# Performance work log

Measured on AMD Instinct MI355X. Metric: run time of the kernel, lower is better.

## Reference

```python
import jax, jax.numpy as jnp
import numpy as np

B, S, D, H = 2, 2048, 1024, 16
HD = D // H  # 64
NUM_BUCKETS = 32
MAX_DISTANCE = 128


def _relative_position_bucket(relative_position, num_buckets=NUM_BUCKETS, max_distance=MAX_DISTANCE):
    # bidirectional=True branch of the torch code
    num_buckets //= 2
    rel_buckets = (relative_position > 0).astype(jnp.int32) * num_buckets
    rp = jnp.abs(relative_position)
    max_exact = num_buckets // 2
    is_small = rp < max_exact
    # log-spaced buckets for larger distances
    rp_large = max_exact + (
        jnp.log(rp.astype(jnp.float32) / max_exact)
        / np.log(max_distance / max_exact)
        * (num_buckets - max_exact)
    ).astype(jnp.int32)
    rp_large = jnp.minimum(rp_large, num_buckets - 1)
    return rel_buckets + jnp.where(is_small, rp, rp_large)


def compute_bias(rel_bias, query_length, key_length):
    ctx = jnp.arange(query_length)[:, None]
    mem = jnp.arange(key_length)[None, :]
    buckets = _relative_position_bucket(mem - ctx)  # [q, k]
    values = rel_bias[buckets]                      # [q, k, h]
    return jnp.transpose(values, (2, 0, 1))[None]   # [1, h, q, k]


def setup_inputs() -> dict:
    key = jax.random.key(0)
    ks = jax.random.split(key, 6)
    scale = 1.0 / np.sqrt(D)
    return {
        "hidden_states": jax.random.normal(ks[0], (B, S, D), jnp.float32),
        "mask": jnp.ones((B, 1, 1, S), jnp.int32),
        "Wq": jax.random.normal(ks[1], (D, D), jnp.float32) * scale,
        "Wk": jax.random.normal(ks[2], (D, D), jnp.float32) * scale,
        "Wv": jax.random.normal(ks[3], (D, D), jnp.float32) * scale,
        "Wo": jax.random.normal(ks[4], (D, D), jnp.float32) * scale,
        "rel_bias": jax.random.normal(ks[5], (NUM_BUCKETS, H), jnp.float32),
    }


def reference(hidden_states, mask, Wq, Wk, Wv, Wo, rel_bias):
    b, s, _ = hidden_states.shape
    # projections (no bias), split heads -> [b, h, s, hd]
    def proj(x, W):
        return jnp.einsum("bsd,ed->bse", x, W).reshape(b, s, H, HD).transpose(0, 2, 1, 3)
    q = proj(hidden_states, Wq)
    k = proj(hidden_states, Wk)
    v = proj(hidden_states, Wv)
    # unscaled attention scores (T5 style): [b, h, s, s]
    scores = jnp.einsum("bhqd,bhkd->bhqk", q, k)
    position_bias = compute_bias(rel_bias, s, s)
    scores = scores + position_bias
    scores = jnp.where(mask == 0, jnp.float32(-1e9), scores)
    attn_weights = jax.nn.softmax(scores, axis=-1)
    # dropout p=0.0 (eval): identity
    attn_output = jnp.einsum("bhqk,bhkd->bhqd", attn_weights, v)
    attn_output = attn_output.transpose(0, 2, 1, 3).reshape(b, s, H * HD)
    attn_output = jnp.einsum("bse,de->bsd", attn_output, Wo)
    return attn_output, attn_weights, position_bias
```

## Files before the change

kernel.cpp:

```cpp
#include <hip/hip_runtime.h>

typedef __attribute__((ext_vector_type(8))) _Float16 half8;
typedef __attribute__((ext_vector_type(4))) _Float16 half4;
typedef __attribute__((ext_vector_type(4))) float f32x4;

#define SEQ 2048
#define DMODEL 1024
#define NHEAD 16
#define HEADD 64
#define NBH 32
#define LUTW 4096

__device__ __forceinline__ void nt_store_f4(float* p, f32x4 v) {
    __builtin_nontemporal_store(v, (f32x4*)p);
}

#define LDS_BAR() do {                                   \
    __builtin_amdgcn_sched_barrier(0);                   \
    asm volatile("s_waitcnt lgkmcnt(0)" ::: "memory");   \
    __builtin_amdgcn_sched_barrier(0);                   \
    __builtin_amdgcn_s_barrier();                        \
    __builtin_amdgcn_sched_barrier(0);                   \
} while (0)

__device__ __forceinline__ int rel_bucket(int rel) {
    int ret = (rel > 0) ? 16 : 0;
    int rp = rel < 0 ? -rel : rel;
    if (rp < 8) return ret + rp;
    float x = logf((float)rp * 0.125f) / 2.7725887f * 8.0f;
    int v = 8 + (int)x;
    v = v < 15 ? v : 15;
    return ret + v;
}

__global__ __launch_bounds__(256) void prep_kernel(const float* __restrict__ hs,
                                                   const float* __restrict__ Wq,
                                                   const float* __restrict__ Wk,
                                                   const float* __restrict__ Wv,
                                                   const float* __restrict__ Wo,
                                                   const float* __restrict__ rel_bias,
                                                   _Float16* __restrict__ Xh,
                                                   _Float16* __restrict__ Wqh,
                                                   _Float16* __restrict__ Wkh,
                                                   _Float16* __restrict__ Wvh,
                                                   _Float16* __restrict__ Woh,
                                                   float* __restrict__ lut) {
    int bid = blockIdx.x;
    if (bid < 4096) {
        const float* in;
        _Float16* out;
        int base;
        if (bid < 2048)      { in = hs; out = Xh;  base = bid; }
        else if (bid < 2560) { in = Wq; out = Wqh; base = bid - 2048; }
        else if (bid < 3072) { in = Wk; out = Wkh; base = bid - 2560; }
        else if (bid < 3584) { in = Wv; out = Wvh; base = bid - 3072; }
        else                 { in = Wo; out = Woh; base = bid - 3584; }
        int i = (base * 256 + threadIdx.x) * 8;
        f32x4 a = *(const f32x4*)(in + i);
        f32x4 b = *(const f32x4*)(in + i + 4);
        half8 r;
        r[0] = (_Float16)a[0]; r[1] = (_Float16)a[1];
        r[2] = (_Float16)a[2]; r[3] = (_Float16)a[3];
        r[4] = (_Float16)b[0]; r[5] = (_Float16)b[1];
        r[6] = (_Float16)b[2]; r[7] = (_Float16)b[3];
        *(half8*)(out + i) = r;
    } else {
        int i = (bid - 4096) * 256 + threadIdx.x;
        int h = i >> 12;
        int idx = i & (LUTW - 1);
        int rel = idx - 2047;
        int b = rel_bucket(rel);
        lut[i] = rel_bias[b * NHEAD + h];
    }
}

__global__ __launch_bounds__(256) void proj3_kernel(const _Float16* __restrict__ Xh,
                                                    const _Float16* __restrict__ Wqh,
                                                    const _Float16* __restrict__ Wkh,
                                                    const _Float16* __restrict__ Wvh,
                                                    _Float16* __restrict__ Qh,
                                                    _Float16* __restrict__ Kh,
                                                    _Float16* __restrict__ Vt,
                                                    const float* __restrict__ lut,
                                                    float* __restrict__ posb) {
    int z = blockIdx.z;
    if (z == 3) {
        int flat = blockIdx.y * 8 + blockIdx.x;
        const size_t total = (size_t)NHEAD * SEQ * SEQ / 4;
        for (size_t idx = (size_t)flat * 256 + threadIdx.x; idx < total; idx += 65536) {
            size_t e = idx * 4;
            int k = (int)(e & 2047);
            int q = (int)((e >> 11) & 2047);
            int h = (int)(e >> 22);
            f32x4 v;
            __builtin_memcpy(&v, lut + h * LUTW + (k - q + 2047), 16);
            nt_store_f4(posb + e, v);
        }
        return;
    }
    const _Float16* B = (z == 0) ? Wqh : (z == 1) ? Wkh : Wvh;
    int l = threadIdx.x & 63, w = threadIdx.x >> 6;
    int row0 = blockIdx.y * 128 + (w >> 1) * 64;
    int col0 = blockIdx.x * 128 + (w & 1) * 64;
    int ar = l & 15, ak = (l >> 4) * 8;
    f32x4 acc[4][4] = {};
    for (int k0 = 0; k0 < DMODEL; k0 += 32) {
        half8 af[4], bf[4];
#pragma unroll
        for (int mi = 0; mi < 4; mi++)
            af[mi] = *(const half8*)(Xh + (size_t)(row0 + mi * 16 + ar) * DMODEL + k0 + ak);
#pragma unroll
        for (int ni = 0; ni < 4; ni++)
            bf[ni] = *(const half8*)(B + (size_t)(col0 + ni * 16 + ar) * DMODEL + k0 + ak);
#pragma unroll
        for (int mi = 0; mi < 4; mi++)
#pragma unroll
            for (int ni = 0; ni < 4; ni++)
                acc[mi][ni] = __builtin_amdgcn_mfma_f32_16x16x32_f16(af[mi], bf[ni], acc[mi][ni], 0, 0, 0);
    }
    int cr = (l >> 4) * 4, cc = l & 15;
    if (z < 2) {
        _Float16* C = z == 0 ? Qh : Kh;
#pragma unroll
        for (int mi = 0; mi < 4; mi++)
#pragma unroll
            for (int ni = 0; ni < 4; ni++) {
                int c = col0 + ni * 16 + cc;
#pragma unroll
                for (int j = 0; j < 4; j++)
                    C[(size_t)(row0 + mi * 16 + cr + j) * DMODEL + c] = (_Float16)acc[mi][ni][j];
            }
    } else {
#pragma unroll
        for (int mi = 0; mi < 4; mi++)
#pragma unroll
            for (int ni = 0; ni < 4; ni++) {
                int c = col0 + ni * 16 + cc;
                int h = c >> 6, hd = c & 63;
                int r = row0 + mi * 16 + cr;
                int b = r >> 11, s0 = r & 2047;
                half4 pk;
#pragma unroll
                for (int j = 0; j < 4; j++) pk[j] = (_Float16)acc[mi][ni][j];
                *(half4*)(Vt + (size_t)((b * NHEAD + h) * HEADD + hd) * SEQ + s0) = pk;
            }
    }
}

__global__ __launch_bounds__(256) void outgemm_kernel(const _Float16* __restrict__ A,
                                                      const _Float16* __restrict__ B,
                                                      float* __restrict__ C) {
    int l = threadIdx.x & 63, w = threadIdx.x >> 6;
    int row0 = blockIdx.y * 128 + (w >> 1) * 64;
    int col0 = blockIdx.x * 128 + (w & 1) * 64;
    int ar = l & 15, ak = (l >> 4) * 8;
    f32x4 acc[4][4] = {};
    for (int k0 = 0; k0 < DMODEL; k0 += 32) {
        half8 af[4], bf[4];
#pragma unroll
        for (int mi = 0; mi < 4; mi++)
            af[mi] = *(const half8*)(A + (size_t)(row0 + mi * 16 + ar) * DMODEL + k0 + ak);
#pragma unroll
        for (int ni = 0; ni < 4; ni++)
            bf[ni] = *(const half8*)(B + (size_t)(col0 + ni * 16 + ar) * DMODEL + k0 + ak);
#pragma unroll
        for (int mi = 0; mi < 4; mi++)
#pragma unroll
            for (int ni = 0; ni < 4; ni++)
                acc[mi][ni] = __builtin_amdgcn_mfma_f32_16x16x32_f16(af[mi], bf[ni], acc[mi][ni], 0, 0, 0);
    }
    int cr = (l >> 4) * 4, cc = l & 15;
#pragma unroll
    for (int mi = 0; mi < 4; mi++)
#pragma unroll
        for (int ni = 0; ni < 4; ni++) {
            int c = col0 + ni * 16 + cc;
#pragma unroll
            for (int j = 0; j < 4; j++)
                C[(size_t)(row0 + mi * 16 + cr + j) * DMODEL + c] = acc[mi][ni][j];
        }
}

__global__ __launch_bounds__(256) void attn_kernel(const _Float16* __restrict__ Q,
                                                   const _Float16* __restrict__ Kg,
                                                   const _Float16* __restrict__ Vg,
                                                   const float* __restrict__ lut,
                                                   const int* __restrict__ mask,
                                                   float* __restrict__ wts,
                                                   _Float16* __restrict__ attn0) {
    __shared__ _Float16 Kt[64][68];
    __shared__ _Float16 Vl[64][68];
    __shared__ _Float16 Pl[4][16][72];
    int tid = threadIdx.x;
    int l = tid & 63, w = tid >> 6;
    int bid = blockIdx.x;
    int xcd = bid & 7, idx = bid >> 3;
    int bh = (idx >> 4) * 8 + xcd;
    int qpair = idx & 15;
    int b = bh >> 4, h = bh & 15;
    int qbaseA = qpair * 64 + w * 16;
    int qbaseB = qbaseA + 1024;
    size_t hoff = (size_t)(b * SEQ) * DMODEL + h * HEADD;
    int ar = l & 15, g = l >> 4, ak = g * 8;
    const float* luth = lut + h * LUTW;
    float* ob = wts + (size_t)bh * SEQ * SEQ;
    int qA = qbaseA + ar;
    int qB = qbaseB + ar;

    int sr = tid >> 2, sc = (tid & 3) * 16;
    const _Float16* Ksrc = Kg + hoff + sc;
    const _Float16* Vsrc = Vg + ((size_t)bh * HEADD + sr) * SEQ + sc;

    half8 qfA[2], qfB[2];
#pragma unroll
    for (int kk = 0; kk < 2; kk++) {
        qfA[kk] = *(const half8*)(Q + hoff + (size_t)qA * DMODEL + kk * 32 + ak);
        qfB[kk] = *(const half8*)(Q + hoff + (size_t)qB * DMODEL + kk * 32 + ak);
    }

    half8 s0 = *(const half8*)(Ksrc + (size_t)sr * DMODEL);
    half8 s1 = *(const half8*)(Ksrc + (size_t)sr * DMODEL + 8);
    float mA = -3e38f, lsumA = 0.f;
    float mB = -3e38f, lsumB = 0.f;
    for (int k0 = 0; k0 < SEQ; k0 += 64) {
        *(half8*)&Kt[sr][sc] = s0;
        *(half8*)&Kt[sr][sc + 8] = s1;
        LDS_BAR();
        if (k0 + 64 < SEQ) {
            s0 = *(const half8*)(Ksrc + (size_t)(k0 + 64 + sr) * DMODEL);
            s1 = *(const half8*)(Ksrc + (size_t)(k0 + 64 + sr) * DMODEL + 8);
        }
        f32x4 accA[4] = {}, accB[4] = {};
#pragma unroll
        for (int ni = 0; ni < 4; ni++)
#pragma unroll
            for (int kk = 0; kk < 2; kk++) {
                half8 kf = *(const half8*)&Kt[ni * 16 + ar][kk * 32 + ak];
                accA[ni] = __builtin_amdgcn_mfma_f32_16x16x32_f16(kf, qfA[kk], accA[ni], 0, 0, 0);
                accB[ni] = __builtin_amdgcn_mfma_f32_16x16x32_f16(kf, qfB[kk], accB[ni], 0, 0, 0);
            }
        LDS_BAR();
        {
            float vv[16];
#pragma unroll
            for (int ni = 0; ni < 4; ni++) {
                int kcol = k0 + ni * 16 + g * 4;
                int4 mk = *(const int4*)(mask + b * SEQ + kcol);
                const int* mp = (const int*)&mk;
                f32x4 lb4;
                __builtin_memcpy(&lb4, luth + kcol - qA + 2047, 16);
#pragma unroll
                for (int j = 0; j < 4; j++)
                    vv[ni * 4 + j] = mp[j] ? (accA[ni][j] + lb4[j]) : -1e9f;
            }
            float t8[8];
#pragma unroll
            for (int t = 0; t < 8; t++) t8[t] = fmaxf(vv[t], vv[t + 8]);
            float t4a = fmaxf(t8[0], t8[4]), t4b = fmaxf(t8[1], t8[5]);
            float t4c = fmaxf(t8[2], t8[6]), t4d = fmaxf(t8[3], t8[7]);
            float vmax = fmaxf(fmaxf(t4a, t4b), fmaxf(t4c, t4d));
            float mn = fmaxf(mA, vmax);
            float scale = __expf(mA - mn);
            float e[16];
#pragma unroll
            for (int t = 0; t < 16; t++) e[t] = __expf(vv[t] - mn);
            float s8[8];
#pragma unroll
            for (int t = 0; t < 8; t++) s8[t] = e[t] + e[t + 8];
            float s4a = s8[0] + s8[4], s4b = s8[1] + s8[5];
            float s4c = s8[2] + s8[6], s4d = s8[3] + s8[7];
            lsumA = lsumA * scale + (s4a + s4b) + (s4c + s4d);
            mA = mn;
        }
        {
            float vv[16];
#pragma unroll
            for (int ni = 0; ni < 4; ni++) {
                int kcol = k0 + ni * 16 + g * 4;
                int4 mk = *(const int4*)(mask + b * SEQ + kcol);
                const int* mp = (const int*)&mk;
                f32x4 lb4;
                __builtin_memcpy(&lb4, luth + kcol - qB + 2047, 16);
#pragma unroll
                for (int j = 0; j < 4; j++)
                    vv[ni * 4 + j] = mp[j] ? (accB[ni][j] + lb4[j]) : -1e9f;
            }
            float t8[8];
#pragma unroll
            for (int t = 0; t < 8; t++) t8[t] = fmaxf(vv[t], vv[t + 8]);
            float t4a = fmaxf(t8[0], t8[4]), t4b = fmaxf(t8[1], t8[5]);
            float t4c = fmaxf(t8[2], t8[6]), t4d = fmaxf(t8[3], t8[7]);
            float vmax = fmaxf(fmaxf(t4a, t4b), fmaxf(t4c, t4d));
            float mn = fmaxf(mB, vmax);
            float scale = __expf(mB - mn);
            float e[16];
#pragma unroll
            for (int t = 0; t < 16; t++) e[t] = __expf(vv[t] - mn);
            float s8[8];
#pragma unroll
            for (int t = 0; t < 8; t++) s8[t] = e[t] + e[t + 8];
            float s4a = s8[0] + s8[4], s4b = s8[1] + s8[5];
            float s4c = s8[2] + s8[6], s4d = s8[3] + s8[7];
            lsumB = lsumB * scale + (s4a + s4b) + (s4c + s4d);
            mB = mn;
        }
    }
    half8 t0 = *(const half8*)(Ksrc + (size_t)sr * DMODEL);
    half8 t1 = *(const half8*)(Ksrc + (size_t)sr * DMODEL + 8);
    half8 v0 = *(const half8*)(Vsrc);
    half8 v1 = *(const half8*)(Vsrc + 8);
#pragma unroll
    for (int off2 = 16; off2 <= 32; off2 <<= 1) {
        float mo = __shfl_xor(mA, off2);
        float lo = __shfl_xor(lsumA, off2);
        float mn = fmaxf(mA, mo);
        lsumA = lsumA * __expf(mA - mn) + lo * __expf(mo - mn);
        mA = mn;
        mo = __shfl_xor(mB, off2);
        lo = __shfl_xor(lsumB, off2);
        mn = fmaxf(mB, mo);
        lsumB = lsumB * __expf(mB - mn) + lo * __expf(mo - mn);
        mB = mn;
    }
    float invlA = 1.0f / lsumA;
    float invlB = 1.0f / lsumB;
    LDS_BAR();

    f32x4 oaccA[4] = {}, oaccB[4] = {};
    for (int k0 = 0; k0 < SEQ; k0 += 64) {
        *(half8*)&Kt[sr][sc] = t0;
        *(half8*)&Kt[sr][sc + 8] = t1;
        *(half8*)&Vl[sr][sc] = v0;
        *(half8*)&Vl[sr][sc + 8] = v1;
        LDS_BAR();
        if (k0 + 64 < SEQ) {
            t0 = *(const half8*)(Ksrc + (size_t)(k0 + 64 + sr) * DMODEL);
            t1 = *(const half8*)(Ksrc + (size_t)(k0 + 64 + sr) * DMODEL + 8);
            v0 = *(const half8*)(Vsrc + k0 + 64);
            v1 = *(const half8*)(Vsrc + k0 + 64 + 8);
        }
        f32x4 accA[4] = {}, accB[4] = {};
#pragma unroll
        for (int ni = 0; ni < 4; ni++)
#pragma unroll
            for (int kk = 0; kk < 2; kk++) {
                half8 kf = *(const half8*)&Kt[ni * 16 + ar][kk * 32 + ak];
                accA[ni] = __builtin_amdgcn_mfma_f32_16x16x32_f16(kf, qfA[kk], accA[ni], 0, 0, 0);
                accB[ni] = __builtin_amdgcn_mfma_f32_16x16x32_f16(kf, qfB[kk], accB[ni], 0, 0, 0);
            }
#pragma unroll
        for (int ni = 0; ni < 4; ni++) {
            int kcol = k0 + ni * 16 + g * 4;
            int4 mk = *(const int4*)(mask + b * SEQ + kcol);
            const int* mp = (const int*)&mk;
            f32x4 lb4;
            __builtin_memcpy(&lb4, luth + kcol - qA + 2047, 16);
            f32x4 wv;
#pragma unroll
            for (int j = 0; j < 4; j++) {
                float v = mp[j] ? (accA[ni][j] + lb4[j]) : -1e9f;
                wv[j] = __expf(v - mA) * invlA;
            }
            nt_store_f4(ob + (size_t)qA * SEQ + kcol, wv);
            half4 ph;
#pragma unroll
            for (int j = 0; j < 4; j++) ph[j] = (_Float16)wv[j];
            *(half4*)&Pl[w][ar][ni * 16 + g * 4] = ph;
        }
#pragma unroll
        for (int kk2 = 0; kk2 < 2; kk2++) {
            half8 pa = *(half8*)&Pl[w][ar][kk2 * 32 + g * 8];
#pragma unroll
            for (int ni = 0; ni < 4; ni++) {
                half8 vf = *(const half8*)&Vl[ni * 16 + ar][kk2 * 32 + g * 8];
                oaccA[ni] = __builtin_amdgcn_mfma_f32_16x16x32_f16(pa, vf, oaccA[ni], 0, 0, 0);
            }
        }
#pragma unroll
        for (int ni = 0; ni < 4; ni++) {
            int kcol = k0 + ni * 16 + g * 4;
            int4 mk = *(const int4*)(mask + b * SEQ + kcol);
            const int* mp = (const int*)&mk;
            f32x4 lb4;
            __builtin_memcpy(&lb4, luth + kcol - qB + 2047, 16);
            f32x4 wv;
#pragma unroll
            for (int j = 0; j < 4; j++) {
                float v = mp[j] ? (accB[ni][j] + lb4[j]) : -1e9f;
                wv[j] = __expf(v - mB) * invlB;
            }
            nt_store_f4(ob + (size_t)qB * SEQ + kcol, wv);
            half4 ph;
#pragma unroll
            for (int j = 0; j < 4; j++) ph[j] = (_Float16)wv[j];
            *(half4*)&Pl[w][ar][ni * 16 + g * 4] = ph;
        }
#pragma unroll
        for (int kk2 = 0; kk2 < 2; kk2++) {
            half8 pa = *(half8*)&Pl[w][ar][kk2 * 32 + g * 8];
#pragma unroll
            for (int ni = 0; ni < 4; ni++) {
                half8 vf = *(const half8*)&Vl[ni * 16 + ar][kk2 * 32 + g * 8];
                oaccB[ni] = __builtin_amdgcn_mfma_f32_16x16x32_f16(pa, vf, oaccB[ni], 0, 0, 0);
            }
        }
        LDS_BAR();
    }
#pragma unroll
    for (int ni = 0; ni < 4; ni++)
#pragma unroll
        for (int j = 0; j < 4; j++) {
            attn0[(size_t)(b * SEQ + qbaseA + g * 4 + j) * DMODEL + h * HEADD + ni * 16 + ar] =
                (_Float16)oaccA[ni][j];
            attn0[(size_t)(b * SEQ + qbaseB + g * 4 + j) * DMODEL + h * HEADD + ni * 16 + ar] =
                (_Float16)oaccB[ni][j];
        }
}

extern "C" void kernel_launch(void* const* d_in, const int* in_sizes, int n_in,
                              void* d_out, int out_size, void* d_ws, size_t ws_size,
                              hipStream_t stream) {
    const float* hs = (const float*)d_in[0];
    const int* mask = (const int*)d_in[1];
    const float* Wq = (const float*)d_in[2];
    const float* Wk = (const float*)d_in[3];
    const float* Wv = (const float*)d_in[4];
    const float* Wo = (const float*)d_in[5];
    const float* rel_bias = (const float*)d_in[6];

    float* out_attn = (float*)d_out;
    float* out_wts = out_attn + (size_t)2 * SEQ * DMODEL;
    float* out_posb = out_wts + (size_t)NBH * SEQ * SEQ;

    char* ws = (char*)d_ws;
    size_t off = 0;
    auto carve = [&](size_t bytes) { void* p = ws + off; off += (bytes + 255) & ~(size_t)255; return p; };
    _Float16* Xh  = (_Float16*)carve((size_t)2 * SEQ * DMODEL * 2);
    _Float16* Wqh = (_Float16*)carve((size_t)DMODEL * DMODEL * 2);
    _Float16* Wkh = (_Float16*)carve((size_t)DMODEL * DMODEL * 2);
    _Float16* Wvh = (_Float16*)carve((size_t)DMODEL * DMODEL * 2);
    _Float16* Woh = (_Float16*)carve((size_t)DMODEL * DMODEL * 2);
    _Float16* Qh  = (_Float16*)carve((size_t)2 * SEQ * DMODEL * 2);
    _Float16* Kh  = (_Float16*)carve((size_t)2 * SEQ * DMODEL * 2);
    _Float16* Vt  = (_Float16*)carve((size_t)NBH * HEADD * SEQ * 2);
    _Float16* A0h = (_Float16*)carve((size_t)2 * SEQ * DMODEL * 2);
    float* lut    = (float*)carve((size_t)NHEAD * LUTW * 4);

    prep_kernel<<<4352, 256, 0, stream>>>(hs, Wq, Wk, Wv, Wo, rel_bias,
                                          Xh, Wqh, Wkh, Wvh, Woh, lut);

    dim3 pg(DMODEL / 128, (2 * SEQ) / 128, 4);
    proj3_kernel<<<pg, 256, 0, stream>>>(Xh, Wqh, Wkh, Wvh, Qh, Kh, Vt, lut, out_posb);

    attn_kernel<<<512, 256, 0, stream>>>(Qh, Kh, Vt, lut, mask, out_wts, A0h);

    dim3 og(DMODEL / 128, (2 * SEQ) / 128);
    outgemm_kernel<<<og, 256, 0, stream>>>(A0h, Woh, out_attn);
}
```

Baseline: 433.6 us.

## Merge two query-pair blocks into one 512-thread block sharing K/V tiles

The attention kernel now launches 256 blocks of 512 threads instead of 512 blocks of 256. Each block covers two query-pair groups that share the same K and V LDS tiles, which halves the global-to-LDS staging per block and splits each thread's load into a single half8. Mask and position-bias loads are also hoisted right after the barrier so they overlap the QK MFMAs. The trade-offs are fewer blocks in the grid for occupancy and higher register pressure under the 512-thread launch bound.

```diff
diff --git a/kernel.cpp b/kernel.cpp
--- a/kernel.cpp
+++ b/kernel.cpp
@@ -181,7 +181,7 @@
         }
 }
 
-__global__ __launch_bounds__(256) void attn_kernel(const _Float16* __restrict__ Q,
+__global__ __launch_bounds__(512) void attn_kernel(const _Float16* __restrict__ Q,
                                                    const _Float16* __restrict__ Kg,
                                                    const _Float16* __restrict__ Vg,
                                                    const float* __restrict__ lut,
@@ -190,15 +190,16 @@
                                                    _Float16* __restrict__ attn0) {
     __shared__ _Float16 Kt[64][68];
     __shared__ _Float16 Vl[64][68];
-    __shared__ _Float16 Pl[4][16][72];
+    __shared__ _Float16 Pl[8][16][72];
     int tid = threadIdx.x;
-    int l = tid & 63, w = tid >> 6;
+    int l = tid & 63, wid = tid >> 6;
+    int wsub = wid & 3, psel = wid >> 2;
     int bid = blockIdx.x;
     int xcd = bid & 7, idx = bid >> 3;
-    int bh = (idx >> 4) * 8 + xcd;
-    int qpair = idx & 15;
+    int bh = (idx >> 3) * 8 + xcd;
+    int qp = (idx & 7) * 2 + psel;
     int b = bh >> 4, h = bh & 15;
-    int qbaseA = qpair * 64 + w * 16;
+    int qbaseA = qp * 64 + wsub * 16;
     int qbaseB = qbaseA + 1024;
     size_t hoff = (size_t)(b * SEQ) * DMODEL + h * HEADD;
     int ar = l & 15, g = l >> 4, ak = g * 8;
@@ -207,7 +208,7 @@
     int qA = qbaseA + ar;
     int qB = qbaseB + ar;
 
-    int sr = tid >> 2, sc = (tid & 3) * 16;
+    int sr = tid >> 3, sc = (tid & 7) * 8;
     const _Float16* Ksrc = Kg + hoff + sc;
     const _Float16* Vsrc = Vg + ((size_t)bh * HEADD + sr) * SEQ + sc;
 
@@ -219,17 +220,22 @@
     }
 
     half8 s0 = *(const half8*)(Ksrc + (size_t)sr * DMODEL);
-    half8 s1 = *(const half8*)(Ksrc + (size_t)sr * DMODEL + 8);
     float mA = -3e38f, lsumA = 0.f;
     float mB = -3e38f, lsumB = 0.f;
     for (int k0 = 0; k0 < SEQ; k0 += 64) {
         *(half8*)&Kt[sr][sc] = s0;
-        *(half8*)&Kt[sr][sc + 8] = s1;
         LDS_BAR();
-        if (k0 + 64 < SEQ) {
+        int4 mk[4];
+        f32x4 lbA[4], lbB[4];
+#pragma unroll
+        for (int ni = 0; ni < 4; ni++) {
+            int kcol = k0 + ni * 16 + g * 4;
+            mk[ni] = *(const int4*)(mask + b * SEQ + kcol);
+            __builtin_memcpy(&lbA[ni], luth + kcol - qA + 2047, 16);
+            __builtin_memcpy(&lbB[ni], luth + kcol - qB + 2047, 16);
+        }
+        if (k0 + 64 < SEQ)
             s0 = *(const half8*)(Ksrc + (size_t)(k0 + 64 + sr) * DMODEL);
-            s1 = *(const half8*)(Ksrc + (size_t)(k0 + 64 + sr) * DMODEL + 8);
-        }
         f32x4 accA[4] = {}, accB[4] = {};
 #pragma unroll
         for (int ni = 0; ni < 4; ni++)
@@ -244,14 +250,10 @@
             float vv[16];
 #pragma unroll
             for (int ni = 0; ni < 4; ni++) {
-                int kcol = k0 + ni * 16 + g * 4;
-                int4 mk = *(const int4*)(mask + b * SEQ + kcol);
-                const int* mp = (const int*)&mk;
-                f32x4 lb4;
-                __builtin_memcpy(&lb4, luth + kcol - qA + 2047, 16);
+                const int* mp = (const int*)&mk[ni];
 #pragma unroll
                 for (int j = 0; j < 4; j++)
-                    vv[ni * 4 + j] = mp[j] ? (accA[ni][j] + lb4[j]) : -1e9f;
+                    vv[ni * 4 + j] = mp[j] ? (accA[ni][j] + lbA[ni][j]) : -1e9f;
             }
             float t8[8];
 #pragma unroll
@@ -276,14 +278,10 @@
             float vv[16];
 #pragma unroll
             for (int ni = 0; ni < 4; ni++) {
-                int kcol = k0 + ni * 16 + g * 4;
-                int4 mk = *(const int4*)(mask + b * SEQ + kcol);
-                const int* mp = (const int*)&mk;
-                f32x4 lb4;
-                __builtin_memcpy(&lb4, luth + kcol - qB + 2047, 16);
+                const int* mp = (const int*)&mk[ni];
 #pragma unroll
                 for (int j = 0; j < 4; j++)
-                    vv[ni * 4 + j] = mp[j] ? (accB[ni][j] + lb4[j]) : -1e9f;
+                    vv[ni * 4 + j] = mp[j] ? (accB[ni][j] + lbB[ni][j]) : -1e9f;
             }
             float t8[8];
 #pragma unroll
@@ -306,9 +304,7 @@
         }
     }
     half8 t0 = *(const half8*)(Ksrc + (size_t)sr * DMODEL);
-    half8 t1 = *(const half8*)(Ksrc + (size_t)sr * DMODEL + 8);
     half8 v0 = *(const half8*)(Vsrc);
-    half8 v1 = *(const half8*)(Vsrc + 8);
 #pragma unroll
     for (int off2 = 16; off2 <= 32; off2 <<= 1) {
         float mo = __shfl_xor(mA, off2);
@@ -329,15 +325,20 @@
     f32x4 oaccA[4] = {}, oaccB[4] = {};
     for (int k0 = 0; k0 < SEQ; k0 += 64) {
         *(half8*)&Kt[sr][sc] = t0;
-        *(half8*)&Kt[sr][sc + 8] = t1;
         *(half8*)&Vl[sr][sc] = v0;
-        *(half8*)&Vl[sr][sc + 8] = v1;
         LDS_BAR();
+        int4 mk[4];
+        f32x4 lbA[4], lbB[4];
+#pragma unroll
+        for (int ni = 0; ni < 4; ni++) {
+            int kcol = k0 + ni * 16 + g * 4;
+            mk[ni] = *(const int4*)(mask + b * SEQ + kcol);
+            __builtin_memcpy(&lbA[ni], luth + kcol - qA + 2047, 16);
+            __builtin_memcpy(&lbB[ni], luth + kcol - qB + 2047, 16);
+        }
         if (k0 + 64 < SEQ) {
             t0 = *(const half8*)(Ksrc + (size_t)(k0 + 64 + sr) * DMODEL);
-            t1 = *(const half8*)(Ksrc + (size_t)(k0 + 64 + sr) * DMODEL + 8);
             v0 = *(const half8*)(Vsrc + k0 + 64);
-            v1 = *(const half8*)(Vsrc + k0 + 64 + 8);
         }
         f32x4 accA[4] = {}, accB[4] = {};
 #pragma unroll
@@ -351,25 +352,22 @@
 #pragma unroll
         for (int ni = 0; ni < 4; ni++) {
             int kcol = k0 + ni * 16 + g * 4;
-            int4 mk = *(const int4*)(mask + b * SEQ + kcol);
-            const int* mp = (const int*)&mk;
-            f32x4 lb4;
-            __builtin_memcpy(&lb4, luth + kcol - qA + 2047, 16);
+            const int* mp = (const int*)&mk[ni];
             f32x4 wv;
 #pragma unroll
             for (int j = 0; j < 4; j++) {
-                float v = mp[j] ? (accA[ni][j] + lb4[j]) : -1e9f;
+                float v = mp[j] ? (accA[ni][j] + lbA[ni][j]) : -1e9f;
                 wv[j] = __expf(v - mA) * invlA;
             }
             nt_store_f4(ob + (size_t)qA * SEQ + kcol, wv);
             half4 ph;
 #pragma unroll
             for (int j = 0; j < 4; j++) ph[j] = (_Float16)wv[j];
-            *(half4*)&Pl[w][ar][ni * 16 + g * 4] = ph;
+            *(half4*)&Pl[wid][ar][ni * 16 + g * 4] = ph;
         }
 #pragma unroll
         for (int kk2 = 0; kk2 < 2; kk2++) {
-            half8 pa = *(half8*)&Pl[w][ar][kk2 * 32 + g * 8];
+            half8 pa = *(half8*)&Pl[wid][ar][kk2 * 32 + g * 8];
 #pragma unroll
             for (int ni = 0; ni < 4; ni++) {
                 half8 vf = *(const half8*)&Vl[ni * 16 + ar][kk2 * 32 + g * 8];
@@ -379,25 +377,22 @@
 #pragma unroll
         for (int ni = 0; ni < 4; ni++) {
             int kcol = k0 + ni * 16 + g * 4;
-            int4 mk = *(const int4*)(mask + b * SEQ + kcol);
-            const int* mp = (const int*)&mk;
-            f32x4 lb4;
-            __builtin_memcpy(&lb4, luth + kcol - qB + 2047, 16);
+            const int* mp = (const int*)&mk[ni];
             f32x4 wv;
 #pragma unroll
             for (int j = 0; j < 4; j++) {
-                float v = mp[j] ? (accB[ni][j] + lb4[j]) : -1e9f;
+                float v = mp[j] ? (accB[ni][j] + lbB[ni][j]) : -1e9f;
                 wv[j] = __expf(v - mB) * invlB;
             }
             nt_store_f4(ob + (size_t)qB * SEQ + kcol, wv);
             half4 ph;
 #pragma unroll
             for (int j = 0; j < 4; j++) ph[j] = (_Float16)wv[j];
-            *(half4*)&Pl[w][ar][ni * 16 + g * 4] = ph;
+            *(half4*)&Pl[wid][ar][ni * 16 + g * 4] = ph;
         }
 #pragma unroll
         for (int kk2 = 0; kk2 < 2; kk2++) {
-            half8 pa = *(half8*)&Pl[w][ar][kk2 * 32 + g * 8];
+            half8 pa = *(half8*)&Pl[wid][ar][kk2 * 32 + g * 8];
 #pragma unroll
             for (int ni = 0; ni < 4; ni++) {
                 half8 vf = *(const half8*)&Vl[ni * 16 + ar][kk2 * 32 + g * 8];
@@ -452,7 +447,7 @@
     dim3 pg(DMODEL / 128, (2 * SEQ) / 128, 4);
     proj3_kernel<<<pg, 256, 0, stream>>>(Xh, Wqh, Wkh, Wvh, Qh, Kh, Vt, lut, out_posb);
 
-    attn_kernel<<<512, 256, 0, stream>>>(Qh, Kh, Vt, lut, mask, out_wts, A0h);
+    attn_kernel<<<256, 512, 0, stream>>>(Qh, Kh, Vt, lut, mask, out_wts, A0h);
 
     dim3 og(DMODEL / 128, (2 * SEQ) / 128);
     outgemm_kernel<<<og, 256, 0, stream>>>(A0h, Woh, out_attn);
```

Measured after the change: 432.3 us. Within noise of the previous version (-0.3%).
